# Kernel optimization log

Measured on AMD Instinct MI355X. Metric: run time of the kernel, lower is better.

Reference implementation:

```python
import jax, jax.numpy as jnp
import numpy as np

B, L_DEC, V = 8, 256, 32000
L_SRC = 512
V_EXT = 32128


def setup_inputs() -> dict:
    key = jax.random.key(0)
    k1, k2, k3, k4 = jax.random.split(key, 4)
    dist_t = jax.random.uniform(k1, (B, L_DEC, V), dtype=jnp.float32)
    p_gen = jax.random.uniform(k2, (B, L_DEC, 1), dtype=jnp.float32)
    alph_t = jax.random.uniform(k3, (B, L_SRC, L_DEC), dtype=jnp.float32)
    batch_vocab = jnp.zeros((V_EXT,), dtype=jnp.float32)  # only shape[0] is used
    pointer = jax.random.randint(k4, (B, L_SRC), 0, V_EXT, dtype=jnp.int32)
    return {"dist_t": dist_t, "p_gen": p_gen, "alph_t": alph_t,
            "batch_vocab": batch_vocab, "pointer": pointer}


def reference(dist_t, p_gen, alph_t, batch_vocab, pointer):
    v_ext = batch_vocab.shape[0]
    nb, nl, ndim = dist_t.shape
    # p_gen * [vocab ; zeros padding up to extended vocab]
    prob_vocab = p_gen * jnp.pad(dist_t, ((0, 0), (0, 0), (0, v_ext - ndim)))
    # torch builds a dense one-hot [B, L_src, V_ext] and does bmm(alpha^T, one_hot).
    # Mathematically: copyp[b, t, v] = sum_{s : pointer[b,s]==v} alpha[b, s, t]
    # -> scatter-add of attention weights into pointed vocab slots.
    alpha_td = jnp.swapaxes(alph_t, 1, 2)  # [B, L_dec, L_src]

    def scatter_one(a_td, ptr):  # a_td: [L_dec, L_src], ptr: [L_src]
        return jnp.zeros((a_td.shape[0], v_ext), a_td.dtype).at[:, ptr].add(a_td)

    copyp = jax.vmap(scatter_one)(alpha_td, pointer)  # [B, L_dec, V_ext]
    proba = prob_vocab + (1.0 - p_gen) * copyp
    return proba
```

## Files before the change

### kernel.cpp

```cpp
#include <hip/hip_runtime.h>

#define B_     8
#define L_DEC_ 256
#define V_     32000
#define L_SRC_ 512
#define V_EXT_ 32128

#define V4_    (V_ / 4)
#define VE4_   (V_EXT_ / 4)
#define PAD4_  (VE4_ - V4_)

typedef float f32x4 __attribute__((ext_vector_type(4)));

__global__ __launch_bounds__(512, 8) void copynet_fused(
    const float* __restrict__ dist,
    const float* __restrict__ p_gen,
    const float* __restrict__ alph,
    const int*   __restrict__ pointer,
    float* __restrict__ out)
{
    const int row = blockIdx.x;
    const int b   = row >> 8;
    const int t   = row & (L_DEC_ - 1);
    const int tid = threadIdx.x;

    const float pg   = p_gen[row];
    const float coef = 1.0f - pg;

    const int   sIdx = b * L_SRC_ + tid;
    const int   v    = pointer[sIdx];
    const float val  = coef * alph[(size_t)sIdx * L_DEC_ + t];

    const f32x4* dist4 = (const f32x4*)(dist + (size_t)row * V_);
    f32x4*       out4  = (f32x4*)(out + (size_t)row * V_EXT_);

    for (int i = tid; i < V4_; i += 512) {
        f32x4 d = __builtin_nontemporal_load(dist4 + i);
        d *= pg;
        out4[i] = d;
    }
    if (tid < PAD4_) {
        f32x4 z = {0.f, 0.f, 0.f, 0.f};
        out4[V4_ + tid] = z;
    }

    __syncthreads();

    atomicAdd(out + (size_t)row * V_EXT_ + v, val);
}

extern "C" void kernel_launch(void* const* d_in, const int* in_sizes, int n_in,
                              void* d_out, int out_size, void* d_ws, size_t ws_size,
                              hipStream_t stream)
{
    const float* dist    = (const float*)d_in[0];
    const float* p_gen   = (const float*)d_in[1];
    const float* alph    = (const float*)d_in[2];
    const int*   pointer = (const int*)d_in[4];
    float* out = (float*)d_out;

    copynet_fused<<<B_ * L_DEC_, 512, 0, stream>>>(dist, p_gen, alph, pointer, out);
}
```

Measured before the change: 476.7 us.

## Replace global atomic scatter with shared-memory bucketed merge into output stream

Builds per-block linked-list buckets in shared memory, keyed by owner thread (v>>2 mod 512). During the streaming write each thread adds the matching copy probabilities in registers, so the separate global atomicAdd pass and its read-after-write on output are gone. Stores become nontemporal. The cost is extra shared-memory work, an extra barrier and per-iteration list walks with divergent branches. Using nontemporal stores could also change cache behaviour.

```diff
diff --git a/kernel.cpp b/kernel.cpp
--- a/kernel.cpp
+++ b/kernel.cpp
@@ -8,7 +8,7 @@
 
 #define V4_    (V_ / 4)
 #define VE4_   (V_EXT_ / 4)
-#define PAD4_  (VE4_ - V4_)
+#define NITER_ ((VE4_ + 511) / 512)
 
 typedef float f32x4 __attribute__((ext_vector_type(4)));
 
@@ -19,6 +19,11 @@
     const int*   __restrict__ pointer,
     float* __restrict__ out)
 {
+    __shared__ int   head[512];
+    __shared__ int   nxt[512];
+    __shared__ int   key[512];
+    __shared__ float sval[512];
+
     const int row = blockIdx.x;
     const int b   = row >> 8;
     const int t   = row & (L_DEC_ - 1);
@@ -31,22 +36,40 @@
     const int   v    = pointer[sIdx];
     const float val  = coef * alph[(size_t)sIdx * L_DEC_ + t];
 
+    head[tid] = -1;
+    __syncthreads();
+    key[tid]  = v;
+    sval[tid] = val;
+    const int owner = (v >> 2) & 511;
+    nxt[tid] = atomicExch(&head[owner], tid);
+    __syncthreads();
+
+    const int myHead = head[tid];
     const f32x4* dist4 = (const f32x4*)(dist + (size_t)row * V_);
     f32x4*       out4  = (f32x4*)(out + (size_t)row * V_EXT_);
 
-    for (int i = tid; i < V4_; i += 512) {
-        f32x4 d = __builtin_nontemporal_load(dist4 + i);
-        d *= pg;
-        out4[i] = d;
+    for (int k = 0; k < NITER_; ++k) {
+        const int i = tid + (k << 9);
+        if (i >= VE4_) break;
+        f32x4 r;
+        if (i < V4_) {
+            r = __builtin_nontemporal_load(dist4 + i) * pg;
+        } else {
+            r = (f32x4){0.f, 0.f, 0.f, 0.f};
+        }
+        for (int e = myHead; e != -1; e = nxt[e]) {
+            const int kv = key[e];
+            if ((kv >> 2) == i) {
+                const float a = sval[e];
+                const int   c = kv & 3;
+                r.x += (c == 0) ? a : 0.f;
+                r.y += (c == 1) ? a : 0.f;
+                r.z += (c == 2) ? a : 0.f;
+                r.w += (c == 3) ? a : 0.f;
+            }
+        }
+        __builtin_nontemporal_store(r, out4 + i);
     }
-    if (tid < PAD4_) {
-        f32x4 z = {0.f, 0.f, 0.f, 0.f};
-        out4[V4_ + tid] = z;
-    }
-
-    __syncthreads();
-
-    atomicAdd(out + (size_t)row * V_EXT_ + v, val);
 }
 
 extern "C" void kernel_launch(void* const* d_in, const int* in_sizes, int n_in,
```

New measurement: 439.4 us. 1.08x faster.
